# Kernel optimization log

Measured on AMD Instinct MI355X. Metric: run time of the kernel, lower is better.

## Reference

```python
import jax, jax.numpy as jnp
import numpy as np

HIDDEN = 1024
HEADS = 16
HEAD_DIM = HIDDEN // HEADS  # 64; softmax scale uses head_dim per SeqAttention(hidden_size=head_dim)


def setup_inputs() -> dict:
    key = jax.random.key(0)
    ks = jax.random.split(key, 7)
    B, M = 2, 2048
    s = 1.0 / np.sqrt(HIDDEN)
    return {
        "query": jax.random.normal(ks[0], (B, M, HIDDEN), jnp.float32),
        "key": jax.random.normal(ks[1], (B, M, HIDDEN), jnp.float32),
        "value": jax.random.normal(ks[2], (B, M, HIDDEN), jnp.float32),
        "Wq": jax.random.normal(ks[3], (HIDDEN, HIDDEN), jnp.float32) * s,
        "Wk": jax.random.normal(ks[4], (HIDDEN, HIDDEN), jnp.float32) * s,
        "Wv": jax.random.normal(ks[5], (HIDDEN, HIDDEN), jnp.float32) * s,
        "Wo": jax.random.normal(ks[6], (HIDDEN, HIDDEN), jnp.float32) * s,
    }


def _split_heads(x):
    # [B, T, H*D] -> [B, H, T, D]
    B, T, _ = x.shape
    return x.reshape(B, T, HEADS, HEAD_DIM).transpose(0, 2, 1, 3)


def reference(query, key, value, Wq, Wk, Wv, Wo):
    # nn.Linear(bias=False): y = x @ W.T
    q = _split_heads(query @ Wq.T)  # [B,H,M,D]
    k = _split_heads(key @ Wk.T)    # [B,H,N,D]
    v = _split_heads(value @ Wv.T)  # [B,H,N,D]
    scale = 1.0 / jnp.sqrt(jnp.asarray(HEAD_DIM, q.dtype))
    attn = jnp.einsum("bhmd,bhnd->bhmn", q, k) * scale
    attn = jax.nn.softmax(attn, axis=-1)
    out = jnp.einsum("bhmn,bhnd->bhmd", attn, v)  # [B,H,M,D]
    B, H, M, D = out.shape
    out = out.transpose(0, 2, 1, 3).reshape(B, M, H * D)
    return out @ Wo.T
```

## Files before the change

kernel.cpp:

```cpp
#include <hip/hip_runtime.h>

typedef __bf16 bf16;
typedef __bf16 bf16x2 __attribute__((ext_vector_type(2)));
typedef __bf16 bf16x8 __attribute__((ext_vector_type(8)));
typedef float  f32x4  __attribute__((ext_vector_type(4)));
typedef float  f32x16 __attribute__((ext_vector_type(16)));
typedef unsigned int u32;
typedef unsigned int u32x4 __attribute__((ext_vector_type(4)));

typedef __attribute__((address_space(1))) unsigned int gu32;
typedef __attribute__((address_space(3))) unsigned int lu32;

__device__ __forceinline__ void llds16(const void* g, void* l) {
  __builtin_amdgcn_global_load_lds((gu32*)g, (lu32*)l, 16, 0, 0);
}

__device__ __forceinline__ void cvt8(const float* __restrict__ src,
                                     bf16* __restrict__ dst, int i) {
  const float4* s4 = (const float4*)src;
  float4 a = s4[i * 2 + 0];
  float4 c = s4[i * 2 + 1];
  bf16x8 o;
  o[0] = (bf16)a.x; o[1] = (bf16)a.y; o[2] = (bf16)a.z; o[3] = (bf16)a.w;
  o[4] = (bf16)c.x; o[5] = (bf16)c.y; o[6] = (bf16)c.z; o[7] = (bf16)c.w;
  ((bf16x8*)dst)[i] = o;
}

__global__ __launch_bounds__(256) void cvt_bf16(const float* __restrict__ src,
                                                bf16* __restrict__ dst, int n8) {
  int i = blockIdx.x * blockDim.x + threadIdx.x;
  if (i < n8) cvt8(src, dst, i);
}

__global__ __launch_bounds__(256) void cvt_all(const float* __restrict__ w0,
                                               const float* __restrict__ w1,
                                               const float* __restrict__ w2,
                                               const float* __restrict__ w3,
                                               const float* __restrict__ x0,
                                               const float* __restrict__ x1,
                                               const float* __restrict__ x2,
                                               bf16* __restrict__ wdst,
                                               bf16* __restrict__ xdst) {
  const int b = blockIdx.x;
  if (b < 2048) {
    const int which = b >> 9;
    const float* src = (which == 0) ? w0 : (which == 1) ? w1 : (which == 2) ? w2 : w3;
    const int i = (b & 511) * 256 + threadIdx.x;
    cvt8(src, wdst + (size_t)which * (1u << 20), i);
  } else {
    const int b2 = b - 2048;
    const int which = b2 >> 11;
    const float* src = (which == 0) ? x0 : (which == 1) ? x1 : x2;
    const int i = (b2 & 2047) * 256 + threadIdx.x;
    cvt8(src, xdst + (size_t)which * (4u << 20), i);
  }
}

__global__ __launch_bounds__(256) void gemm_qkv(const bf16* __restrict__ A0,
                                                const bf16* __restrict__ A1,
                                                const bf16* __restrict__ A2,
                                                const bf16* __restrict__ Wb,
                                                bf16* __restrict__ qb,
                                                bf16* __restrict__ kb,
                                                bf16* __restrict__ vb,
                                                int zoff) {
  constexpr int K = 1024, BM = 128, BN = 128, BK = 32, NT = K / BK;
  __shared__ bf16 Alds[2][BM * BK];
  __shared__ bf16 Blds[2][BN * BK];
  const int t = threadIdx.x, w = t >> 6, l = t & 63;
  const int lr = l & 15, lg = l >> 4;
  const int bm = blockIdx.x * BM, bn = blockIdx.y * BN;
  const int z = blockIdx.z + zoff;
  const bf16* A = (z == 0) ? A0 : (z == 1) ? A1 : A2;
  const bf16* W = Wb + (size_t)z * (1u << 20);
  const int wm = (w >> 1) * 64, wn = (w & 1) * 64;

  f32x4 acc[4][4] = {};

  auto stage = [&](int buf, int kt) {
    const int k0 = kt * BK;
#pragma unroll
    for (int i = 0; i < 2; ++i) {
      int idx = i * 256 + t;
      int p = idx >> 3, q = idx & 7;
      int c = q ^ (p & 7);
      llds16((const char*)A + ((size_t)(bm + 2 * p + (c >> 2)) * K + k0) * 2 + (c & 3) * 16,
             (char*)(&Alds[buf][0]) + (i * 4 + w) * 1024);
    }
#pragma unroll
    for (int i = 0; i < 2; ++i) {
      int idx = i * 256 + t;
      int p = idx >> 3, q = idx & 7;
      int c = q ^ (p & 7);
      llds16((const char*)W + ((size_t)(bn + 2 * p + (c >> 2)) * K + k0) * 2 + (c & 3) * 16,
             (char*)(&Blds[buf][0]) + (i * 4 + w) * 1024);
    }
  };

  stage(0, 0);
  for (int kt = 0; kt < NT; ++kt) {
    __syncthreads();
    if (kt + 1 < NT) stage((kt + 1) & 1, kt + 1);
    const int cur = kt & 1;
    bf16x8 af[4], bfr[4];
#pragma unroll
    for (int i = 0; i < 4; ++i) {
      const int row = wm + i * 16 + lr;
      const int p = row >> 1, h = row & 1;
      af[i] = *(const bf16x8*)((const char*)(&Alds[cur][0]) + p * 128 +
                               (((h * 4 + lg) ^ (p & 7)) * 16));
    }
#pragma unroll
    for (int j = 0; j < 4; ++j) {
      const int row = wn + j * 16 + lr;
      const int p = row >> 1, h = row & 1;
      bfr[j] = *(const bf16x8*)((const char*)(&Blds[cur][0]) + p * 128 +
                                (((h * 4 + lg) ^ (p & 7)) * 16));
    }
    __builtin_amdgcn_s_setprio(1);
#pragma unroll
    for (int i = 0; i < 4; ++i)
#pragma unroll
      for (int j = 0; j < 4; ++j)
        acc[i][j] = __builtin_amdgcn_mfma_f32_16x16x32_bf16(af[i], bfr[j], acc[i][j], 0, 0, 0);
    __builtin_amdgcn_s_setprio(0);
  }

  bf16* Cout = (z == 0) ? qb : (z == 1) ? kb : vb;
  const float osc = (z == 0) ? 0.1803368801f : 1.0f;
#pragma unroll
  for (int i = 0; i < 4; ++i) {
#pragma unroll
    for (int j = 0; j < 4; ++j) {
#pragma unroll
      for (int r = 0; r < 4; ++r) {
        const int gm = bm + wm + i * 16 + lg * 4 + r;
        const int n  = bn + wn + j * 16 + lr;
        const int b = gm >> 11, m = gm & 2047;
        const int h = n >> 6, d = n & 63;
        const size_t off = (z < 2)
            ? ((size_t)((b * 16 + h) * 2048 + m) * 64 + d)
            : ((size_t)((b * 16 + h) * 64 + d) * 2048 + m);
        Cout[off] = (bf16)(acc[i][j][r] * osc);
      }
    }
  }
}

__global__ __launch_bounds__(256) void gemm_out(const bf16* __restrict__ A,
                                                const bf16* __restrict__ Bw,
                                                float* __restrict__ Cout) {
  constexpr int N = 1024, K = 1024;
  constexpr int BM = 128, BN = 64, BK = 64, NT = K / BK;
  __shared__ bf16 Alds[2][BM * BK];
  __shared__ bf16 Blds[2][BN * BK];
  const int t = threadIdx.x;
  const int w = t >> 6, l = t & 63;
  const int lr = l & 15, lg = l >> 4;
  const int bm = blockIdx.x * BM, bn = blockIdx.y * BN;
  const int wm = (w >> 1) * 64, wn = (w & 1) * 32;
  const int key = (lr & 7) << 4;

  f32x4 acc[4][2] = {};

  auto stage = [&](int buf, int kt) {
    const int k0 = kt * BK;
#pragma unroll
    for (int i = 0; i < 4; ++i) {
      int idx = i * 256 + t;
      int row = idx >> 3, c = idx & 7;
      llds16((const char*)A + ((size_t)(bm + row) * K + k0) * 2 + ((c ^ (row & 7)) * 16),
             (char*)(&Alds[buf][0]) + (i * 4 + w) * 1024);
    }
#pragma unroll
    for (int i = 0; i < 2; ++i) {
      int idx = i * 256 + t;
      int row = idx >> 3, c = idx & 7;
      llds16((const char*)Bw + ((size_t)(bn + row) * K + k0) * 2 + ((c ^ (row & 7)) * 16),
             (char*)(&Blds[buf][0]) + (i * 4 + w) * 1024);
    }
  };

  stage(0, 0);
  for (int kt = 0; kt < NT; ++kt) {
    __syncthreads();
    if (kt + 1 < NT) stage((kt + 1) & 1, kt + 1);
    const int cur = kt & 1;
    bf16x8 af[4][2], bfr[2][2];
#pragma unroll
    for (int i = 0; i < 4; ++i) {
      const int row = wm + i * 16 + lr;
      const char* rb = (const char*)(&Alds[cur][0]) + row * 128;
#pragma unroll
      for (int kk = 0; kk < 2; ++kk)
        af[i][kk] = *(const bf16x8*)(rb + ((kk * 64 + lg * 16) ^ key));
    }
#pragma unroll
    for (int j = 0; j < 2; ++j) {
      const int row = wn + j * 16 + lr;
      const char* rb = (const char*)(&Blds[cur][0]) + row * 128;
#pragma unroll
      for (int kk = 0; kk < 2; ++kk)
        bfr[j][kk] = *(const bf16x8*)(rb + ((kk * 64 + lg * 16) ^ key));
    }
    __builtin_amdgcn_s_setprio(1);
#pragma unroll
    for (int kk = 0; kk < 2; ++kk)
#pragma unroll
      for (int i = 0; i < 4; ++i)
#pragma unroll
        for (int j = 0; j < 2; ++j)
          acc[i][j] = __builtin_amdgcn_mfma_f32_16x16x32_bf16(af[i][kk], bfr[j][kk], acc[i][j], 0, 0, 0);
    __builtin_amdgcn_s_setprio(0);
  }

#pragma unroll
  for (int i = 0; i < 4; ++i)
#pragma unroll
    for (int j = 0; j < 2; ++j)
#pragma unroll
      for (int r = 0; r < 4; ++r) {
        const int gm = bm + wm + i * 16 + lg * 4 + r;
        const int n  = bn + wn + j * 16 + lr;
        Cout[(size_t)gm * N + n] = acc[i][j][r];
      }
}

__global__ __launch_bounds__(256) void attn_fwd(const bf16* __restrict__ Qb,
                                                const bf16* __restrict__ Kb,
                                                const bf16* __restrict__ Vt,
                                                bf16* __restrict__ Out) {
  constexpr int Mlen = 2048, KVB = 64, NTT = Mlen / KVB;
  __shared__ bf16 Klds[4][KVB * 64];
  __shared__ bf16 Vlds[4][64 * KVB];
  const int t = threadIdx.x, w = t >> 6, l = t & 63;
  const int l31 = l & 31, hi = l >> 5;
  const int orig = blockIdx.x;
  const int wg = (orig & 7) * 64 + (orig >> 3);
  const int bh = wg >> 4;
  const int qr = (wg & 15) * 128 + w * 32;
  const int key = (l31 & 7) << 4;

  const bf16* qbase = Qb + ((size_t)bh * Mlen + qr + l31) * 64;
  bf16x8 qf[4];
#pragma unroll
  for (int dks = 0; dks < 4; ++dks)
    qf[dks] = *(const bf16x8*)(qbase + dks * 16 + hi * 8);

  u32x4 onesw;
  onesw[0] = 0x3F803F80u; onesw[1] = 0x3F803F80u;
  onesw[2] = 0x3F803F80u; onesw[3] = 0x3F803F80u;
  const bf16x8 ones = __builtin_bit_cast(bf16x8, onesw);

  f32x16 acco0 = {}, acco1 = {};
  f32x16 accl = {};

  const char* kTile0 = (const char*)Kb + (size_t)bh * Mlen * 64 * 2;
  const char* vBase  = (const char*)Vt + (size_t)bh * 64 * Mlen * 2;

  auto stageKV = [&](int buf, int tile) {
    const int kv0 = tile * KVB;
#pragma unroll
    for (int i = 0; i < 2; ++i) {
      int idx = i * 256 + t;
      int L = idx * 16;
      int row = L >> 7;
      int inner = (L & 127) ^ ((row & 7) << 4);
      llds16(kTile0 + (size_t)(kv0 + row) * 128 + inner,
             (char*)(&Klds[buf][0]) + (i * 4 + w) * 1024);
    }
#pragma unroll
    for (int i = 0; i < 2; ++i) {
      int idx = i * 256 + t;
      int L = idx * 16;
      int d = L >> 7;
      int inner = (L & 127) ^ ((d & 7) << 4);
      llds16(vBase + (size_t)d * (Mlen * 2) + kv0 * 2 + inner,
             (char*)(&Vlds[buf][0]) + (i * 4 + w) * 1024);
    }
  };

  auto STEP_HEAD = [&](int tile) {
    if (tile + 1 < NTT) {
      stageKV((tile + 1) & 3, tile + 1);
      asm volatile("s_waitcnt vmcnt(4)" ::: "memory");
    } else {
      asm volatile("s_waitcnt vmcnt(0)" ::: "memory");
    }
    __builtin_amdgcn_s_barrier();
    __builtin_amdgcn_sched_barrier(0);
  };
  auto QK = [&](int tile, f32x16& s0, f32x16& s1) {
    const char* kb_ = (const char*)(&Klds[tile & 3][0]);
    __builtin_amdgcn_s_setprio(1);
#pragma unroll
    for (int dks = 0; dks < 4; ++dks) {
      const int a0 = (0 * 32 + l31) * 128 + ((dks * 32 + hi * 16) ^ key);
      const int a1 = (1 * 32 + l31) * 128 + ((dks * 32 + hi * 16) ^ key);
      bf16x8 kf0 = *(const bf16x8*)(kb_ + a0);
      bf16x8 kf1 = *(const bf16x8*)(kb_ + a1);
      s0 = __builtin_amdgcn_mfma_f32_32x32x16_bf16(kf0, qf[dks], s0, 0, 0, 0);
      s1 = __builtin_amdgcn_mfma_f32_32x32x16_bf16(kf1, qf[dks], s1, 0, 0, 0);
    }
    __builtin_amdgcn_s_setprio(0);
  };
  auto EXP = [&](const f32x16& s0, const f32x16& s1, u32 (&w0)[8], u32 (&w1)[8]) {
#pragma unroll
    for (int e2 = 0; e2 < 8; ++e2) {
      const float p00 = __builtin_amdgcn_exp2f(s0[2 * e2]);
      const float p01 = __builtin_amdgcn_exp2f(s0[2 * e2 + 1]);
      const float p10 = __builtin_amdgcn_exp2f(s1[2 * e2]);
      const float p11 = __builtin_amdgcn_exp2f(s1[2 * e2 + 1]);
      bf16x2 k0; k0[0] = (bf16)p00; k0[1] = (bf16)p01;
      bf16x2 k1; k1[0] = (bf16)p10; k1[1] = (bf16)p11;
      w0[e2] = __builtin_bit_cast(u32, k0);
      w1[e2] = __builtin_bit_cast(u32, k1);
    }
  };
  auto PV = [&](int tprev, const u32 (&w0)[8], const u32 (&w1)[8]) {
    const char* vb_ = (const char*)(&Vlds[tprev & 3][0]);
    __builtin_amdgcn_s_setprio(1);
#pragma unroll
    for (int ks = 0; ks < 2; ++ks) {
      auto sa0 = __builtin_amdgcn_permlane32_swap(w0[4 * ks + 0], w0[4 * ks + 2], false, false);
      auto sa1 = __builtin_amdgcn_permlane32_swap(w0[4 * ks + 1], w0[4 * ks + 3], false, false);
      auto sb0 = __builtin_amdgcn_permlane32_swap(w1[4 * ks + 0], w1[4 * ks + 2], false, false);
      auto sb1 = __builtin_amdgcn_permlane32_swap(w1[4 * ks + 1], w1[4 * ks + 3], false, false);
      u32x4 fa, fb;
      fa[0] = (u32)sa0[0]; fa[1] = (u32)sa1[0]; fa[2] = (u32)sa0[1]; fa[3] = (u32)sa1[1];
      fb[0] = (u32)sb0[0]; fb[1] = (u32)sb1[0]; fb[2] = (u32)sb0[1]; fb[3] = (u32)sb1[1];
      const bf16x8 pa = __builtin_bit_cast(bf16x8, fa);
      const bf16x8 pb = __builtin_bit_cast(bf16x8, fb);
      const int c0 = (ks * 32 + hi * 16);
      bf16x8 va0 = *(const bf16x8*)(vb_ + (0 * 32 + l31) * 128 + ((0 * 64 + c0) ^ key));
      bf16x8 va1 = *(const bf16x8*)(vb_ + (1 * 32 + l31) * 128 + ((0 * 64 + c0) ^ key));
      bf16x8 vb0 = *(const bf16x8*)(vb_ + (0 * 32 + l31) * 128 + ((1 * 64 + c0) ^ key));
      bf16x8 vb1 = *(const bf16x8*)(vb_ + (1 * 32 + l31) * 128 + ((1 * 64 + c0) ^ key));
      acco0 = __builtin_amdgcn_mfma_f32_32x32x16_bf16(pa, va0, acco0, 0, 0, 0);
      acco1 = __builtin_amdgcn_mfma_f32_32x32x16_bf16(pa, va1, acco1, 0, 0, 0);
      accl  = __builtin_amdgcn_mfma_f32_32x32x16_bf16(pa, ones, accl, 0, 0, 0);
      acco0 = __builtin_amdgcn_mfma_f32_32x32x16_bf16(pb, vb0, acco0, 0, 0, 0);
      acco1 = __builtin_amdgcn_mfma_f32_32x32x16_bf16(pb, vb1, acco1, 0, 0, 0);
      accl  = __builtin_amdgcn_mfma_f32_32x32x16_bf16(pb, ones, accl, 0, 0, 0);
    }
    __builtin_amdgcn_s_setprio(0);
  };

  u32 wE0[8], wE1[8], wO0[8], wO1[8];
  f32x16 s0, s1;

  stageKV(0, 0);
  STEP_HEAD(0);
  s0 = f32x16{}; s1 = f32x16{};
  QK(0, s0, s1);
  EXP(s0, s1, wE0, wE1);
  for (int tp = 0; tp < 15; ++tp) {
    const int to = 2 * tp + 1;
    STEP_HEAD(to);
    s0 = f32x16{}; s1 = f32x16{};
    QK(to, s0, s1);
    PV(to - 1, wE0, wE1);
    EXP(s0, s1, wO0, wO1);
    const int te = to + 1;
    STEP_HEAD(te);
    s0 = f32x16{}; s1 = f32x16{};
    QK(te, s0, s1);
    PV(te - 1, wO0, wO1);
    EXP(s0, s1, wE0, wE1);
  }
  STEP_HEAD(31);
  s0 = f32x16{}; s1 = f32x16{};
  QK(31, s0, s1);
  PV(30, wE0, wE1);
  EXP(s0, s1, wO0, wO1);
  PV(31, wO0, wO1);

  const int b = bh >> 4, h = bh & 15;
#pragma unroll
  for (int e = 0; e < 16; ++e) {
    const int ql = (e & 3) + 8 * (e >> 2) + 4 * hi;
    const float iv = 1.0f / accl[e];
    const size_t row = (size_t)(b * 2048 + qr + ql) * 1024 + h * 64;
    Out[row + l31]      = (bf16)(acco0[e] * iv);
    Out[row + 32 + l31] = (bf16)(acco1[e] * iv);
  }
}

extern "C" void kernel_launch(void* const* d_in, const int* in_sizes, int n_in,
                              void* d_out, int out_size, void* d_ws, size_t ws_size,
                              hipStream_t stream) {
  const float* q  = (const float*)d_in[0];
  const float* k  = (const float*)d_in[1];
  const float* v  = (const float*)d_in[2];
  const float* Wq = (const float*)d_in[3];
  const float* Wk = (const float*)d_in[4];
  const float* Wv = (const float*)d_in[5];
  const float* Wo = (const float*)d_in[6];

  char* ws = (char*)d_ws;
  const dim3 cb(256);

  if (ws_size >= ((size_t)56 << 20)) {
    bf16* Wb = (bf16*)ws;
    bf16* Xq = (bf16*)(ws + (8u  << 20));
    bf16* Xk = (bf16*)(ws + (16u << 20));
    bf16* Xv = (bf16*)(ws + (24u << 20));
    bf16* qb = (bf16*)(ws + (32u << 20));
    bf16* kb = (bf16*)(ws + (40u << 20));
    bf16* vb = (bf16*)(ws + (48u << 20));
    bf16* Xa = (bf16*)(ws + (8u  << 20));

    cvt_all<<<8192, cb, 0, stream>>>(Wq, Wk, Wv, Wo, q, k, v, Wb, Xq);
    gemm_qkv<<<dim3(32, 8, 3), cb, 0, stream>>>(Xq, Xk, Xv, Wb, qb, kb, vb, 0);
    attn_fwd<<<512, cb, 0, stream>>>(qb, kb, vb, Xa);
    gemm_out<<<dim3(32, 16), cb, 0, stream>>>(Xa, Wb + 3 * (1u << 20), (float*)d_out);
  } else {
    bf16* Wb = (bf16*)ws;
    bf16* X  = (bf16*)(ws + (8u  << 20));
    bf16* qb = (bf16*)(ws + (16u << 20));
    bf16* kb = (bf16*)(ws + (24u << 20));
    bf16* vb = (bf16*)(ws + (32u << 20));
    bf16* Xa = (bf16*)(ws + (8u  << 20));

    cvt_all<<<2048, cb, 0, stream>>>(Wq, Wk, Wv, Wo, q, k, v, Wb, Wb);
    cvt_bf16<<<2048, cb, 0, stream>>>(q, X, 524288);
    gemm_qkv<<<dim3(32, 8, 1), cb, 0, stream>>>(X, X, X, Wb, qb, kb, vb, 0);
    cvt_bf16<<<2048, cb, 0, stream>>>(k, X, 524288);
    gemm_qkv<<<dim3(32, 8, 1), cb, 0, stream>>>(X, X, X, Wb, qb, kb, vb, 1);
    cvt_bf16<<<2048, cb, 0, stream>>>(v, X, 524288);
    gemm_qkv<<<dim3(32, 8, 1), cb, 0, stream>>>(X, X, X, Wb, qb, kb, vb, 2);
    attn_fwd<<<512, cb, 0, stream>>>(qb, kb, vb, Xa);
    gemm_out<<<dim3(32, 16), cb, 0, stream>>>(Xa, Wb + 3 * (1u << 20), (float*)d_out);
  }
}
```

Measured before the change: 120.6 us.

## Triple-buffer LDS in projection GEMMs with vmcnt-based partial waits

Both projection GEMMs move from double to triple LDS buffering. Instead of a full __syncthreads before issuing the next stage, each iteration issues the next tile's global-to-LDS loads first, then waits only for the older tile with s_waitcnt vmcnt(N), then barriers. This lets one tile's load stay in flight during compute and uses a single barrier per iteration. In exchange it raises LDS use, which may reduce occupancy, and correctness depends on the hand-picked vmcnt counts matching the number of loads issued per stage.

```diff
diff --git a/kernel.cpp b/kernel.cpp
--- a/kernel.cpp
+++ b/kernel.cpp
@@ -65,8 +65,8 @@
                                                 bf16* __restrict__ vb,
                                                 int zoff) {
   constexpr int K = 1024, BM = 128, BN = 128, BK = 32, NT = K / BK;
-  __shared__ bf16 Alds[2][BM * BK];
-  __shared__ bf16 Blds[2][BN * BK];
+  __shared__ bf16 Alds[3][BM * BK];
+  __shared__ bf16 Blds[3][BN * BK];
   const int t = threadIdx.x, w = t >> 6, l = t & 63;
   const int lr = l & 15, lg = l >> 4;
   const int bm = blockIdx.x * BM, bn = blockIdx.y * BN;
@@ -98,23 +98,30 @@
   };
 
   stage(0, 0);
+  int bufc = 0;
   for (int kt = 0; kt < NT; ++kt) {
-    __syncthreads();
-    if (kt + 1 < NT) stage((kt + 1) & 1, kt + 1);
-    const int cur = kt & 1;
+    const int bufn = (bufc == 2) ? 0 : bufc + 1;
+    if (kt + 1 < NT) {
+      stage(bufn, kt + 1);
+      asm volatile("s_waitcnt vmcnt(4)" ::: "memory");
+    } else {
+      asm volatile("s_waitcnt vmcnt(0)" ::: "memory");
+    }
+    __builtin_amdgcn_s_barrier();
+    __builtin_amdgcn_sched_barrier(0);
     bf16x8 af[4], bfr[4];
 #pragma unroll
     for (int i = 0; i < 4; ++i) {
       const int row = wm + i * 16 + lr;
       const int p = row >> 1, h = row & 1;
-      af[i] = *(const bf16x8*)((const char*)(&Alds[cur][0]) + p * 128 +
+      af[i] = *(const bf16x8*)((const char*)(&Alds[bufc][0]) + p * 128 +
                                (((h * 4 + lg) ^ (p & 7)) * 16));
     }
 #pragma unroll
     for (int j = 0; j < 4; ++j) {
       const int row = wn + j * 16 + lr;
       const int p = row >> 1, h = row & 1;
-      bfr[j] = *(const bf16x8*)((const char*)(&Blds[cur][0]) + p * 128 +
+      bfr[j] = *(const bf16x8*)((const char*)(&Blds[bufc][0]) + p * 128 +
                                 (((h * 4 + lg) ^ (p & 7)) * 16));
     }
     __builtin_amdgcn_s_setprio(1);
@@ -124,6 +131,7 @@
       for (int j = 0; j < 4; ++j)
         acc[i][j] = __builtin_amdgcn_mfma_f32_16x16x32_bf16(af[i], bfr[j], acc[i][j], 0, 0, 0);
     __builtin_amdgcn_s_setprio(0);
+    bufc = bufn;
   }
 
   bf16* Cout = (z == 0) ? qb : (z == 1) ? kb : vb;
@@ -152,8 +160,8 @@
                                                 float* __restrict__ Cout) {
   constexpr int N = 1024, K = 1024;
   constexpr int BM = 128, BN = 64, BK = 64, NT = K / BK;
-  __shared__ bf16 Alds[2][BM * BK];
-  __shared__ bf16 Blds[2][BN * BK];
+  __shared__ bf16 Alds[3][BM * BK];
+  __shared__ bf16 Blds[3][BN * BK];
   const int t = threadIdx.x;
   const int w = t >> 6, l = t & 63;
   const int lr = l & 15, lg = l >> 4;
@@ -182,15 +190,22 @@
   };
 
   stage(0, 0);
+  int bufc = 0;
   for (int kt = 0; kt < NT; ++kt) {
-    __syncthreads();
-    if (kt + 1 < NT) stage((kt + 1) & 1, kt + 1);
-    const int cur = kt & 1;
+    const int bufn = (bufc == 2) ? 0 : bufc + 1;
+    if (kt + 1 < NT) {
+      stage(bufn, kt + 1);
+      asm volatile("s_waitcnt vmcnt(6)" ::: "memory");
+    } else {
+      asm volatile("s_waitcnt vmcnt(0)" ::: "memory");
+    }
+    __builtin_amdgcn_s_barrier();
+    __builtin_amdgcn_sched_barrier(0);
     bf16x8 af[4][2], bfr[2][2];
 #pragma unroll
     for (int i = 0; i < 4; ++i) {
       const int row = wm + i * 16 + lr;
-      const char* rb = (const char*)(&Alds[cur][0]) + row * 128;
+      const char* rb = (const char*)(&Alds[bufc][0]) + row * 128;
 #pragma unroll
       for (int kk = 0; kk < 2; ++kk)
         af[i][kk] = *(const bf16x8*)(rb + ((kk * 64 + lg * 16) ^ key));
@@ -198,7 +213,7 @@
 #pragma unroll
     for (int j = 0; j < 2; ++j) {
       const int row = wn + j * 16 + lr;
-      const char* rb = (const char*)(&Blds[cur][0]) + row * 128;
+      const char* rb = (const char*)(&Blds[bufc][0]) + row * 128;
 #pragma unroll
       for (int kk = 0; kk < 2; ++kk)
         bfr[j][kk] = *(const bf16x8*)(rb + ((kk * 64 + lg * 16) ^ key));
@@ -212,6 +227,7 @@
         for (int j = 0; j < 2; ++j)
           acc[i][j] = __builtin_amdgcn_mfma_f32_16x16x32_bf16(af[i][kk], bfr[j][kk], acc[i][j], 0, 0, 0);
     __builtin_amdgcn_s_setprio(0);
+    bufc = bufn;
   }
 
 #pragma unroll
```

Result: no change. 118.9 us, median of 3 (-1.4%).
